# Kernel optimization log

Hardware: AMD Instinct MI355X
Metric: run time of the kernel (lower is better)

## Reference

```python
import jax, jax.numpy as jnp
import numpy as np
import math

EPS = 1e-5  # torch LayerNorm default


def entmax15(z):
    # Peters & Martins exact sort-based alpha=1.5 entmax along last axis.
    z = z / 2.0
    z = z - jnp.max(z, axis=-1, keepdims=True)
    zs = -jnp.sort(-z, axis=-1)                      # descending
    K = z.shape[-1]
    rho = jnp.arange(1, K + 1, dtype=z.dtype)
    mean = jnp.cumsum(zs, axis=-1) / rho
    mean_sq = jnp.cumsum(zs * zs, axis=-1) / rho
    ss = rho * (mean_sq - mean * mean)
    delta = jnp.clip((1.0 - ss) / rho, 0.0)
    tau = mean - jnp.sqrt(delta)
    k = jnp.sum(tau <= zs, axis=-1, keepdims=True)   # support size
    tau_star = jnp.take_along_axis(tau, k - 1, axis=-1)
    p = jnp.square(jnp.clip(z - tau_star, 0.0))
    return p


def mish(x):
    return x * jnp.tanh(jax.nn.softplus(x))


def layer_norm(x, g, b):
    mu = jnp.mean(x, axis=-1, keepdims=True)
    var = jnp.var(x, axis=-1, keepdims=True)
    return (x - mu) / jnp.sqrt(var + EPS) * g + b


def setup_inputs() -> dict:
    key = jax.random.key(0)
    D, H, F = 512, 8, 2048
    B, S = 8, 1024
    ks = jax.random.split(key, 16)
    s = 1.0 / math.sqrt(D)
    inp = {
        "x": jax.random.normal(ks[0], (B, S, D), jnp.float32),
        # weights stored [in, out]; y = x @ W + b
        "Wq": jax.random.normal(ks[1], (D, D), jnp.float32) * s,
        "bq": jnp.zeros((D,), jnp.float32),
        "Wk": jax.random.normal(ks[2], (D, D), jnp.float32) * s,
        "bk": jnp.zeros((D,), jnp.float32),
        "Wv": jax.random.normal(ks[3], (D, D), jnp.float32) * s,
        "bv": jnp.zeros((D,), jnp.float32),
        "Wo": jax.random.normal(ks[4], (D, D), jnp.float32) * s,
        "bo": jnp.zeros((D,), jnp.float32),
        "g1": jnp.ones((D,), jnp.float32),
        "be1": jnp.zeros((D,), jnp.float32),
        "W1": jax.random.normal(ks[5], (D, F), jnp.float32) * s,
        "b1": jnp.zeros((F,), jnp.float32),
        "W2": jax.random.normal(ks[6], (F, D), jnp.float32) * (1.0 / math.sqrt(F)),
        "b2": jnp.zeros((D,), jnp.float32),
        "g2": jnp.ones((D,), jnp.float32),
        "be2": jnp.zeros((D,), jnp.float32),
    }
    return inp


def reference(x, Wq, bq, Wk, bk, Wv, bv, Wo, bo, g1, be1, W1, b1, W2, b2, g2, be2):
    B, S, D = x.shape
    H = 8
    hd = D // H
    # multi-head self-attention (z = x)
    q = (x @ Wq + bq).reshape(B, S, H, hd).transpose(0, 2, 1, 3)
    k = (x @ Wk + bk).reshape(B, S, H, hd).transpose(0, 2, 1, 3)
    v = (x @ Wv + bv).reshape(B, S, H, hd).transpose(0, 2, 1, 3)
    scores = jnp.einsum("bhqd,bhkd->bhqk", q, k) / math.sqrt(hd)
    attn = entmax15(scores)
    out = jnp.einsum("bhqk,bhkd->bhqd", attn, v)
    out = out.transpose(0, 2, 1, 3).reshape(B, S, D)
    y = out @ Wo + bo
    x = x + layer_norm(y, g1, be1)
    # feed-forward with Mish
    y = mish(x @ W1 + b1) @ W2 + b2
    x = x + layer_norm(y, g2, be2)
    return x
```

## Files before the change

### kernel.cpp

```cpp
#include <hip/hip_runtime.h>


typedef float f32x4 __attribute__((ext_vector_type(4)));
typedef float f32x2 __attribute__((ext_vector_type(2)));
typedef __bf16 b8 __attribute__((ext_vector_type(8)));

#define DEV static __device__ __forceinline__

DEV unsigned short f2bf(float f) {
  unsigned u = __float_as_uint(f);
  u += 0x7fffu + ((u >> 16) & 1u);
  return (unsigned short)(u >> 16);
}
DEV float bf2f(unsigned short b) { return __uint_as_float(((unsigned)b) << 16); }

DEV float mishf(float x) {
  if (x > 20.f) return x;
  float e = __expf(x);
  float u = 1.f + e;
  u *= u;
  return x * ((u - 1.f) / (u + 1.f));
}

DEV void async16(const void* g, void* l) {
  __builtin_amdgcn_global_load_lds(
      (const __attribute__((address_space(1))) unsigned int*)g,
      (__attribute__((address_space(3))) unsigned int*)l, 16, 0, 0);
}

template <int WM, int WN, int EPI, bool OUTBF>
__global__ __launch_bounds__(256) void gemm_bt(
    const unsigned short* __restrict__ A, const unsigned short* __restrict__ Bt,
    const float* __restrict__ bias, void* __restrict__ Cp,
    int K, int lda, int ldb, int ldc,
    long sA1, long sA2, long sB1, long sB2, long sC1, long sC2,
    int hdiv, float alpha) {
  constexpr int BM = WM * 64, BN = WN * 64;
  constexpr int NA = WM * 2, NB = WN * 2;
  __shared__ unsigned short smA[BM * 64];
  __shared__ unsigned short smB[BN * 64];

  const int tid = threadIdx.x;
  const int lane = tid & 63;
  const int z = blockIdx.z;
  const long zi = z / hdiv, zr = z % hdiv;
  const unsigned short* Ab = A + zi * sA1 + zr * sA2 + (long)blockIdx.x * BM * lda;
  const unsigned short* Bb = Bt + zi * sB1 + zr * sB2 + (long)blockIdx.y * BN * ldb;

  int siA[NA];
  const unsigned short* gA[NA];
#pragma unroll
  for (int q = 0; q < NA; ++q) {
    int si = q * 256 + tid;
    int m = si >> 3, s = si & 7, g = s ^ (m & 7);
    siA[q] = si;
    gA[q] = Ab + (long)m * lda + g * 8;
  }
  int siB[NB];
  const unsigned short* gB[NB];
#pragma unroll
  for (int q = 0; q < NB; ++q) {
    int si = q * 256 + tid;
    int m = si >> 3, s = si & 7, g = s ^ (m & 7);
    siB[q] = si;
    gB[q] = Bb + (long)m * ldb + g * 8;
  }

  const int w = tid >> 6;
  const int wr = w / WN, wc = w % WN;
  const int fm = lane & 15, fg = lane >> 4;

  int aOff[4][2], bOff[4][2];
#pragma unroll
  for (int i = 0; i < 4; ++i)
#pragma unroll
    for (int ks = 0; ks < 2; ++ks) {
      int m = wr * 64 + i * 16 + fm;
      aOff[i][ks] = (m * 8 + ((ks * 4 + fg) ^ (fm & 7))) * 8;
      int n = wc * 64 + i * 16 + fm;
      bOff[i][ks] = (n * 8 + ((ks * 4 + fg) ^ (fm & 7))) * 8;
    }

  f32x4 acc[4][4];
#pragma unroll
  for (int i = 0; i < 4; ++i)
#pragma unroll
    for (int j = 0; j < 4; ++j) acc[i][j] = (f32x4){0.f, 0.f, 0.f, 0.f};

  for (int k0 = 0; k0 < K; k0 += 64) {
    __syncthreads();
#pragma unroll
    for (int q = 0; q < NA; ++q) async16(gA[q] + k0, (void*)&smA[siA[q] * 8]);
#pragma unroll
    for (int q = 0; q < NB; ++q) async16(gB[q] + k0, (void*)&smB[siB[q] * 8]);
    __syncthreads();

#pragma unroll
    for (int ks = 0; ks < 2; ++ks) {
      b8 aF[4], bF[4];
#pragma unroll
      for (int i = 0; i < 4; ++i) aF[i] = *(const b8*)&smA[aOff[i][ks]];
#pragma unroll
      for (int j = 0; j < 4; ++j) bF[j] = *(const b8*)&smB[bOff[j][ks]];
#pragma unroll
      for (int i = 0; i < 4; ++i)
#pragma unroll
        for (int j = 0; j < 4; ++j)
          acc[i][j] = __builtin_amdgcn_mfma_f32_16x16x32_bf16(aF[i], bF[j], acc[i][j], 0, 0, 0);
    }
  }

  const long cbase = zi * sC1 + zr * sC2;
  const int row0 = blockIdx.x * BM + wr * 64 + fg * 4;
  const int col0 = blockIdx.y * BN + wc * 64 + fm;
#pragma unroll
  for (int i = 0; i < 4; ++i) {
#pragma unroll
    for (int j = 0; j < 4; ++j) {
      const int col = col0 + j * 16;
      float bv = (EPI >= 1) ? bias[col] : 0.f;
#pragma unroll
      for (int r = 0; r < 4; ++r) {
        const int row = row0 + i * 16 + r;
        float v = acc[i][j][r] * alpha + bv;
        if (EPI == 2) v = mishf(v);
        const long idx = cbase + (long)row * ldc + col;
        if constexpr (OUTBF)
          ((unsigned short*)Cp)[idx] = f2bf(v);
        else
          ((float*)Cp)[idx] = v;
      }
    }
  }
}

__global__ __launch_bounds__(256) void entmax_rows(unsigned short* __restrict__ P) {
  const int tid = threadIdx.x, lane = tid & 63, wv = tid >> 6;
  const long row = (long)blockIdx.x * 4 + wv;
  unsigned short* p = P + row * 1024;

  union { uint4 v; unsigned short u[8]; } a, b;
  a.v = *(const uint4*)(p + lane * 16);
  b.v = *(const uint4*)(p + lane * 16 + 8);
  f32x2 zp[8];
#pragma unroll
  for (int i = 0; i < 4; ++i) {
    zp[i] = (f32x2){bf2f(a.u[2 * i]), bf2f(a.u[2 * i + 1])};
    zp[4 + i] = (f32x2){bf2f(b.u[2 * i]), bf2f(b.u[2 * i + 1])};
  }

  f32x2 mv = zp[0];
#pragma unroll
  for (int i = 1; i < 8; ++i) mv = __builtin_elementwise_max(mv, zp[i]);
  float m = fmaxf(mv.x, mv.y);
#pragma unroll
  for (int o = 32; o; o >>= 1) m = fmaxf(m, __shfl_xor(m, o));

  float tau = m - 1.f;
  int kprev = -1;
  const f32x2 zero2 = (f32x2){0.f, 0.f};
  for (int it = 0; it < 12; ++it) {
    const f32x2 t2 = (f32x2){tau, tau};
    f32x2 s1v = zero2, s2v = zero2;
    int k = 0;
#pragma unroll
    for (int i = 0; i < 8; ++i) {
      f32x2 h = zp[i] - t2;
      k += __popcll(__ballot(h.x > 0.f));
      k += __popcll(__ballot(h.y > 0.f));
      f32x2 hp = __builtin_elementwise_max(h, zero2);
      s1v += hp;
      s2v += hp * hp;
    }
    float s1 = s1v.x + s1v.y, s2 = s2v.x + s2v.y;
#pragma unroll
    for (int o = 32; o; o >>= 1) {
      s1 += __shfl_xor(s1, o);
      s2 += __shfl_xor(s2, o);
    }
    if (k == kprev) break;
    kprev = k;
    float kf = (float)k;
    float disc = fmaxf(fmaf(s1, s1, -kf * (s2 - 1.f)), 0.f);
    tau += (s1 - __builtin_sqrtf(disc)) / kf;
  }

  const f32x2 t2 = (f32x2){tau, tau};
#pragma unroll
  for (int i = 0; i < 4; ++i) {
    f32x2 h0 = __builtin_elementwise_max(zp[i] - t2, zero2);
    f32x2 h1 = __builtin_elementwise_max(zp[4 + i] - t2, zero2);
    f32x2 p0 = h0 * h0, p1 = h1 * h1;
    a.u[2 * i] = f2bf(p0.x);
    a.u[2 * i + 1] = f2bf(p0.y);
    b.u[2 * i] = f2bf(p1.x);
    b.u[2 * i + 1] = f2bf(p1.y);
  }
  *(uint4*)(p + lane * 16) = a.v;
  *(uint4*)(p + lane * 16 + 8) = b.v;
}

__global__ __launch_bounds__(256) void prep_all(
    const float* __restrict__ x, unsigned short* __restrict__ xb,
    const float* __restrict__ Wq, const float* __restrict__ Wk,
    const float* __restrict__ Wv, const float* __restrict__ Wo,
    const float* __restrict__ W1, const float* __restrict__ W2,
    unsigned short* __restrict__ Wqkvt, unsigned short* __restrict__ Wot,
    unsigned short* __restrict__ W1t, unsigned short* __restrict__ W2t,
    const float* __restrict__ bq, const float* __restrict__ bk,
    const float* __restrict__ bv, float* __restrict__ bqkv) {
  __shared__ float t[32][33];
  const int bid = blockIdx.x, tid = threadIdx.x;

  if (bid < 4096) {
    long i = ((long)bid * 256 + tid) * 4;
    float4 v = *(const float4*)&x[i];
    uint2 pk;
    pk.x = (unsigned)f2bf(v.x) | ((unsigned)f2bf(v.y) << 16);
    pk.y = (unsigned)f2bf(v.z) | ((unsigned)f2bf(v.w) << 16);
    *(uint2*)&xb[i] = pk;
    return;
  }

  const float* in;
  unsigned short* out;
  int ldi, ldo, bx, by;
  if (bid < 5120) {
    int t4 = (bid - 4096) >> 8, local = (bid - 4096) & 255;
    const float* ins[4] = {Wq, Wk, Wv, Wo};
    unsigned short* outs[4] = {Wqkvt, Wqkvt + 512 * 512, Wqkvt + 2 * 512 * 512, Wot};
    in = ins[t4];
    out = outs[t4];
    ldi = 512;
    ldo = 512;
    bx = local & 15;
    by = local >> 4;
  } else if (bid < 6144) {
    int local = bid - 5120;
    in = W1;
    out = W1t;
    ldi = 2048;
    ldo = 512;
    bx = local & 63;
    by = local >> 6;
  } else if (bid < 7168) {
    int local = bid - 6144;
    in = W2;
    out = W2t;
    ldi = 512;
    ldo = 2048;
    bx = local & 15;
    by = local >> 4;
  } else {
    int i = (bid - 7168) * 256 + tid;
    if (i < 512) bqkv[i] = bq[i];
    else if (i < 1024) bqkv[i] = bk[i - 512];
    else if (i < 1536) bqkv[i] = bv[i - 1024];
    return;
  }

  const int tx = tid & 31, ty = tid >> 5;
  const int r0 = by * 32, c0 = bx * 32;
#pragma unroll
  for (int q = 0; q < 4; ++q) {
    int r = ty + q * 8;
    t[r][tx] = in[(long)(r0 + r) * ldi + c0 + tx];
  }
  __syncthreads();
#pragma unroll
  for (int q = 0; q < 4; ++q) {
    int r = ty + q * 8;
    out[(long)(c0 + r) * ldo + r0 + tx] = f2bf(t[tx][r]);
  }
}

__global__ __launch_bounds__(256) void transpose_b2b(const unsigned short* __restrict__ in,
                                                     unsigned short* __restrict__ out,
                                                     int ldi, int ldo, long i1, long i2,
                                                     long o1, long o2, int hdiv) {
  __shared__ unsigned short t[32][33];
  const int z = blockIdx.z;
  in += (long)(z / hdiv) * i1 + (long)(z % hdiv) * i2;
  out += (long)(z / hdiv) * o1 + (long)(z % hdiv) * o2;
  const int tx = threadIdx.x & 31, ty = threadIdx.x >> 5;
  const int r0 = blockIdx.y * 32, c0 = blockIdx.x * 32;
#pragma unroll
  for (int q = 0; q < 4; ++q) {
    int r = ty + q * 8;
    t[r][tx] = in[(long)(r0 + r) * ldi + c0 + tx];
  }
  __syncthreads();
#pragma unroll
  for (int q = 0; q < 4; ++q) {
    int r = ty + q * 8;
    out[(long)(c0 + r) * ldo + r0 + tx] = t[tx][r];
  }
}

template <bool WB, int NS>
__global__ __launch_bounds__(256) void ln_res(const float* __restrict__ xin,
                                              const float* __restrict__ y, long ystr,
                                              const float* __restrict__ ybias,
                                              const float* __restrict__ g,
                                              const float* __restrict__ be,
                                              float* __restrict__ xo,
                                              unsigned short* __restrict__ xob) {
  const int row = blockIdx.x, tid = threadIdx.x, lane = tid & 63, wv = tid >> 6;
  const long base = (long)row * 512 + tid * 2;
  const int c = tid * 2;
  float2 v = *(const float2*)&y[base];
#pragma unroll
  for (int j = 1; j < NS; ++j) {
    float2 u = *(const float2*)&y[base + j * ystr];
    v.x += u.x;
    v.y += u.y;
  }
  v.x += ybias[c];
  v.y += ybias[c + 1];
  float s1 = v.x + v.y, s2 = v.x * v.x + v.y * v.y;
  for (int o = 32; o; o >>= 1) {
    s1 += __shfl_xor(s1, o);
    s2 += __shfl_xor(s2, o);
  }
  __shared__ float red[4][2];
  if (lane == 0) {
    red[wv][0] = s1;
    red[wv][1] = s2;
  }
  __syncthreads();
  s1 = red[0][0] + red[1][0] + red[2][0] + red[3][0];
  s2 = red[0][1] + red[1][1] + red[2][1] + red[3][1];
  const float mu = s1 * (1.f / 512.f);
  const float rstd = rsqrtf(s2 * (1.f / 512.f) - mu * mu + 1e-5f);
  float2 xv = *(const float2*)&xin[base];
  float o0 = xv.x + (v.x - mu) * rstd * g[c] + be[c];
  float o1 = xv.y + (v.y - mu) * rstd * g[c + 1] + be[c + 1];
  float2 ov;
  ov.x = o0;
  ov.y = o1;
  *(float2*)&xo[base] = ov;
  if constexpr (WB) {
    unsigned pk = (unsigned)f2bf(o0) | ((unsigned)f2bf(o1) << 16);
    *(unsigned*)&xob[base] = pk;
  }
}

extern "C" void kernel_launch(void* const* d_in, const int* in_sizes, int n_in,
                              void* d_out, int out_size, void* d_ws, size_t ws_size,
                              hipStream_t stream) {
  const int B = 8, S = 1024, D = 512, H = 8, F = 2048;
  const int BS = B * S;
  const int N3 = 3 * D;

  const float* x = (const float*)d_in[0];
  const float* Wq = (const float*)d_in[1];
  const float* bq = (const float*)d_in[2];
  const float* Wk = (const float*)d_in[3];
  const float* bk = (const float*)d_in[4];
  const float* Wv = (const float*)d_in[5];
  const float* bv = (const float*)d_in[6];
  const float* Wo = (const float*)d_in[7];
  const float* bo = (const float*)d_in[8];
  const float* g1 = (const float*)d_in[9];
  const float* be1 = (const float*)d_in[10];
  const float* W1 = (const float*)d_in[11];
  const float* b1 = (const float*)d_in[12];
  const float* W2 = (const float*)d_in[13];
  const float* b2 = (const float*)d_in[14];
  const float* g2 = (const float*)d_in[15];
  const float* be2 = (const float*)d_in[16];
  float* out = (float*)d_out;

  char* w = (char*)d_ws;
  size_t off = 0;
  auto alloc = [&](size_t bytes) -> void* {
    void* p = w + off;
    off += bytes;
    off = (off + 255) & ~(size_t)255;
    return p;
  };

  unsigned short* xb = (unsigned short*)alloc((size_t)BS * D * 2);
  unsigned short* Wqkvt = (unsigned short*)alloc((size_t)N3 * D * 2);
  unsigned short* Wot = (unsigned short*)alloc((size_t)D * D * 2);
  unsigned short* W1t = (unsigned short*)alloc((size_t)F * D * 2);
  unsigned short* W2t = (unsigned short*)alloc((size_t)D * F * 2);
  float* bqkv = (float*)alloc((size_t)N3 * 4);
  unsigned short* QKVb = (unsigned short*)alloc((size_t)BS * N3 * 2);
  unsigned short* Vt = (unsigned short*)alloc((size_t)BS * D * 2);
  unsigned short* attn = (unsigned short*)alloc((size_t)BS * D * 2);
  unsigned short* P = (unsigned short*)alloc((size_t)B * H * S * S * 2);
  float* x1 = (float*)alloc((size_t)BS * D * 4);
  unsigned short* hb = (unsigned short*)alloc((size_t)BS * F * 2);
  unsigned short* x1b = xb;
  float* yp = (float*)P;
  const long PSTR = (long)BS * D;

  const long SS = (long)S * S;
  const long HSS = (long)H * SS;

  prep_all<<<7174, 256, 0, stream>>>(x, xb, Wq, Wk, Wv, Wo, W1, W2,
                                     Wqkvt, Wot, W1t, W2t, bq, bk, bv, bqkv);

  gemm_bt<2, 2, 1, true><<<dim3(BS / 128, N3 / 128, 1), 256, 0, stream>>>(
      xb, Wqkvt, bqkv, QKVb, D, D, D, N3, 0, 0, 0, 0, 0, 0, 1, 1.f);

  transpose_b2b<<<dim3(2, 32, 64), 256, 0, stream>>>(
      QKVb + 1024, Vt, N3, S, (long)S * N3, 64, (long)8 * 64 * S, (long)64 * S, 8);

  gemm_bt<2, 2, 0, true><<<dim3(S / 128, S / 128, B * H), 256, 0, stream>>>(
      QKVb, QKVb + 512, nullptr, P, 64, N3, N3, S,
      (long)S * N3, 64, (long)S * N3, 64, HSS, SS, H, 1.f / 16.f);

  entmax_rows<<<(B * H * S) / 4, 256, 0, stream>>>(P);

  gemm_bt<4, 1, 0, true><<<dim3(S / 256, 1, B * H), 256, 0, stream>>>(
      P, Vt, nullptr, attn, S, S, S, D,
      HSS, SS, (long)8 * 64 * S, (long)64 * S, (long)S * D, 64, H, 1.f);

  gemm_bt<2, 2, 0, false><<<dim3(BS / 128, D / 128, 2), 256, 0, stream>>>(
      attn, Wot, nullptr, yp, D / 2, D, D, D, 0, D / 2, 0, D / 2, 0, PSTR, 2, 1.f);

  ln_res<true, 2><<<BS, 256, 0, stream>>>(x, yp, PSTR, bo, g1, be1, x1, x1b);

  gemm_bt<2, 2, 2, true><<<dim3(BS / 128, F / 128, 1), 256, 0, stream>>>(
      x1b, W1t, b1, hb, D, D, D, F, 0, 0, 0, 0, 0, 0, 1, 1.f);

  gemm_bt<2, 2, 0, false><<<dim3(BS / 128, D / 128, 2), 256, 0, stream>>>(
      hb, W2t, nullptr, yp, F / 2, F, F, D, 0, F / 2, 0, F / 2, 0, PSTR, 2, 1.f);

  ln_res<false, 2><<<BS, 256, 0, stream>>>(x1, yp, PSTR, b2, g2, be2, out, nullptr);
}
```

Before: 355.0 us.

## Swap GEMM operands to store 4-wide vectors; pack two entmax rows per wave

Every GEMM launch now computes the transposed product by swapping its A/B operands and grid axes. Each MFMA lane's four accumulator rows then map to contiguous output columns and can be written with one 8-byte or 16-byte store instead of four scalar stores. The bias is read as a float4 indexed by the new row dimension. The entmax kernel now handles two 1024-wide rows per wavefront, 32 lanes each, with per-half ballot counts and reductions, halving the block count and loading 32 elements per lane. Risks include the bias/layout remapping being correct only because of the swap, and the entmax loop running until both halves converge.

```diff
diff --git a/kernel.cpp b/kernel.cpp
--- a/kernel.cpp
+++ b/kernel.cpp
@@ -115,20 +115,33 @@
   const int col0 = blockIdx.y * BN + wc * 64 + fm;
 #pragma unroll
   for (int i = 0; i < 4; ++i) {
+    const int rowb = row0 + i * 16;
+    float4 bb = make_float4(0.f, 0.f, 0.f, 0.f);
+    if (EPI >= 1) bb = *(const float4*)&bias[rowb];
 #pragma unroll
     for (int j = 0; j < 4; ++j) {
       const int col = col0 + j * 16;
-      float bv = (EPI >= 1) ? bias[col] : 0.f;
-#pragma unroll
-      for (int r = 0; r < 4; ++r) {
-        const int row = row0 + i * 16 + r;
-        float v = acc[i][j][r] * alpha + bv;
-        if (EPI == 2) v = mishf(v);
-        const long idx = cbase + (long)row * ldc + col;
-        if constexpr (OUTBF)
-          ((unsigned short*)Cp)[idx] = f2bf(v);
-        else
-          ((float*)Cp)[idx] = v;
+      const long idx = cbase + (long)col * ldc + rowb;
+      float v0 = acc[i][j][0] * alpha + bb.x;
+      float v1 = acc[i][j][1] * alpha + bb.y;
+      float v2 = acc[i][j][2] * alpha + bb.z;
+      float v3 = acc[i][j][3] * alpha + bb.w;
+      if (EPI == 2) {
+        v0 = mishf(v0);
+        v1 = mishf(v1);
+        v2 = mishf(v2);
+        v3 = mishf(v3);
+      }
+      if constexpr (OUTBF) {
+        ushort4 pk;
+        pk.x = f2bf(v0);
+        pk.y = f2bf(v1);
+        pk.z = f2bf(v2);
+        pk.w = f2bf(v3);
+        *(ushort4*)&((unsigned short*)Cp)[idx] = pk;
+      } else {
+        float4 fv = make_float4(v0, v1, v2, v3);
+        *(float4*)&((float*)Cp)[idx] = fv;
       }
     }
   }
@@ -136,68 +149,71 @@
 
 __global__ __launch_bounds__(256) void entmax_rows(unsigned short* __restrict__ P) {
   const int tid = threadIdx.x, lane = tid & 63, wv = tid >> 6;
-  const long row = (long)blockIdx.x * 4 + wv;
-  unsigned short* p = P + row * 1024;
-
-  union { uint4 v; unsigned short u[8]; } a, b;
-  a.v = *(const uint4*)(p + lane * 16);
-  b.v = *(const uint4*)(p + lane * 16 + 8);
-  f32x2 zp[8];
-#pragma unroll
-  for (int i = 0; i < 4; ++i) {
-    zp[i] = (f32x2){bf2f(a.u[2 * i]), bf2f(a.u[2 * i + 1])};
-    zp[4 + i] = (f32x2){bf2f(b.u[2 * i]), bf2f(b.u[2 * i + 1])};
-  }
+  const int half = lane >> 5, l5 = lane & 31;
+  const long row = (long)blockIdx.x * 8 + wv * 2 + half;
+  unsigned short* p = P + row * 1024 + l5 * 32;
+
+  union { uint4 v; unsigned short u[8]; } t[4];
+#pragma unroll
+  for (int q = 0; q < 4; ++q) t[q].v = *(const uint4*)(p + q * 8);
+  f32x2 zp[16];
+#pragma unroll
+  for (int q = 0; q < 4; ++q)
+#pragma unroll
+    for (int i = 0; i < 4; ++i)
+      zp[q * 4 + i] = (f32x2){bf2f(t[q].u[2 * i]), bf2f(t[q].u[2 * i + 1])};
 
   f32x2 mv = zp[0];
 #pragma unroll
-  for (int i = 1; i < 8; ++i) mv = __builtin_elementwise_max(mv, zp[i]);
+  for (int i = 1; i < 16; ++i) mv = __builtin_elementwise_max(mv, zp[i]);
   float m = fmaxf(mv.x, mv.y);
 #pragma unroll
-  for (int o = 32; o; o >>= 1) m = fmaxf(m, __shfl_xor(m, o));
+  for (int o = 16; o; o >>= 1) m = fmaxf(m, __shfl_xor(m, o));
 
   float tau = m - 1.f;
-  int kprev = -1;
+  int kApr = -1, kBpr = -1;
   const f32x2 zero2 = (f32x2){0.f, 0.f};
   for (int it = 0; it < 12; ++it) {
     const f32x2 t2 = (f32x2){tau, tau};
     f32x2 s1v = zero2, s2v = zero2;
-    int k = 0;
-#pragma unroll
-    for (int i = 0; i < 8; ++i) {
+    int ka = 0, kb = 0;
+#pragma unroll
+    for (int i = 0; i < 16; ++i) {
       f32x2 h = zp[i] - t2;
-      k += __popcll(__ballot(h.x > 0.f));
-      k += __popcll(__ballot(h.y > 0.f));
+      unsigned long long b0 = __ballot(h.x > 0.f);
+      unsigned long long b1 = __ballot(h.y > 0.f);
+      ka += __popc((unsigned)b0) + __popc((unsigned)b1);
+      kb += __popc((unsigned)(b0 >> 32)) + __popc((unsigned)(b1 >> 32));
       f32x2 hp = __builtin_elementwise_max(h, zero2);
       s1v += hp;
       s2v += hp * hp;
     }
     float s1 = s1v.x + s1v.y, s2 = s2v.x + s2v.y;
 #pragma unroll
-    for (int o = 32; o; o >>= 1) {
+    for (int o = 16; o; o >>= 1) {
       s1 += __shfl_xor(s1, o);
       s2 += __shfl_xor(s2, o);
     }
-    if (k == kprev) break;
-    kprev = k;
-    float kf = (float)k;
+    if (ka == kApr && kb == kBpr) break;
+    kApr = ka;
+    kBpr = kb;
+    float kf = (float)(half ? kb : ka);
     float disc = fmaxf(fmaf(s1, s1, -kf * (s2 - 1.f)), 0.f);
     tau += (s1 - __builtin_sqrtf(disc)) / kf;
   }
 
   const f32x2 t2 = (f32x2){tau, tau};
 #pragma unroll
-  for (int i = 0; i < 4; ++i) {
-    f32x2 h0 = __builtin_elementwise_max(zp[i] - t2, zero2);
-    f32x2 h1 = __builtin_elementwise_max(zp[4 + i] - t2, zero2);
-    f32x2 p0 = h0 * h0, p1 = h1 * h1;
-    a.u[2 * i] = f2bf(p0.x);
-    a.u[2 * i + 1] = f2bf(p0.y);
-    b.u[2 * i] = f2bf(p1.x);
-    b.u[2 * i + 1] = f2bf(p1.y);
-  }
-  *(uint4*)(p + lane * 16) = a.v;
-  *(uint4*)(p + lane * 16 + 8) = b.v;
+  for (int q = 0; q < 4; ++q) {
+#pragma unroll
+    for (int i = 0; i < 4; ++i) {
+      f32x2 h = __builtin_elementwise_max(zp[q * 4 + i] - t2, zero2);
+      f32x2 pr = h * h;
+      t[q].u[2 * i] = f2bf(pr.x);
+      t[q].u[2 * i + 1] = f2bf(pr.y);
+    }
+    *(uint4*)(p + q * 8) = t[q].v;
+  }
 }
 
 __global__ __launch_bounds__(256) void prep_all(
@@ -398,36 +414,37 @@
 
   const long SS = (long)S * S;
   const long HSS = (long)H * SS;
+  const long SN3 = (long)S * N3;
 
   prep_all<<<7174, 256, 0, stream>>>(x, xb, Wq, Wk, Wv, Wo, W1, W2,
                                      Wqkvt, Wot, W1t, W2t, bq, bk, bv, bqkv);
 
-  gemm_bt<2, 2, 1, true><<<dim3(BS / 128, N3 / 128, 1), 256, 0, stream>>>(
-      xb, Wqkvt, bqkv, QKVb, D, D, D, N3, 0, 0, 0, 0, 0, 0, 1, 1.f);
+  gemm_bt<2, 2, 1, true><<<dim3(N3 / 128, BS / 128, 1), 256, 0, stream>>>(
+      Wqkvt, xb, bqkv, QKVb, D, D, D, N3, 0, 0, 0, 0, 0, 0, 1, 1.f);
 
   transpose_b2b<<<dim3(2, 32, 64), 256, 0, stream>>>(
-      QKVb + 1024, Vt, N3, S, (long)S * N3, 64, (long)8 * 64 * S, (long)64 * S, 8);
+      QKVb + 1024, Vt, N3, S, SN3, 64, (long)8 * 64 * S, (long)64 * S, 8);
 
   gemm_bt<2, 2, 0, true><<<dim3(S / 128, S / 128, B * H), 256, 0, stream>>>(
-      QKVb, QKVb + 512, nullptr, P, 64, N3, N3, S,
-      (long)S * N3, 64, (long)S * N3, 64, HSS, SS, H, 1.f / 16.f);
-
-  entmax_rows<<<(B * H * S) / 4, 256, 0, stream>>>(P);
-
-  gemm_bt<4, 1, 0, true><<<dim3(S / 256, 1, B * H), 256, 0, stream>>>(
-      P, Vt, nullptr, attn, S, S, S, D,
-      HSS, SS, (long)8 * 64 * S, (long)64 * S, (long)S * D, 64, H, 1.f);
-
-  gemm_bt<2, 2, 0, false><<<dim3(BS / 128, D / 128, 2), 256, 0, stream>>>(
-      attn, Wot, nullptr, yp, D / 2, D, D, D, 0, D / 2, 0, D / 2, 0, PSTR, 2, 1.f);
+      QKVb + 512, QKVb, nullptr, P, 64, N3, N3, S,
+      SN3, 64, SN3, 64, HSS, SS, H, 1.f / 16.f);
+
+  entmax_rows<<<(B * H * S) / 8, 256, 0, stream>>>(P);
+
+  gemm_bt<1, 4, 0, true><<<dim3(1, S / 256, B * H), 256, 0, stream>>>(
+      Vt, P, nullptr, attn, S, S, S, D,
+      (long)8 * 64 * S, (long)64 * S, HSS, SS, (long)S * D, 64, H, 1.f);
+
+  gemm_bt<2, 2, 0, false><<<dim3(D / 128, BS / 128, 2), 256, 0, stream>>>(
+      Wot, attn, nullptr, yp, D / 2, D, D, D, 0, D / 2, 0, D / 2, 0, PSTR, 2, 1.f);
 
   ln_res<true, 2><<<BS, 256, 0, stream>>>(x, yp, PSTR, bo, g1, be1, x1, x1b);
 
-  gemm_bt<2, 2, 2, true><<<dim3(BS / 128, F / 128, 1), 256, 0, stream>>>(
-      x1b, W1t, b1, hb, D, D, D, F, 0, 0, 0, 0, 0, 0, 1, 1.f);
-
-  gemm_bt<2, 2, 0, false><<<dim3(BS / 128, D / 128, 2), 256, 0, stream>>>(
-      hb, W2t, nullptr, yp, F / 2, F, F, D, 0, F / 2, 0, F / 2, 0, PSTR, 2, 1.f);
+  gemm_bt<2, 2, 2, true><<<dim3(F / 128, BS / 128, 1), 256, 0, stream>>>(
+      W1t, x1b, b1, hb, D, D, D, F, 0, 0, 0, 0, 0, 0, 1, 1.f);
+
+  gemm_bt<2, 2, 0, false><<<dim3(D / 128, BS / 128, 2), 256, 0, stream>>>(
+      W2t, hb, nullptr, yp, F / 2, F, F, D, 0, F / 2, 0, F / 2, 0, PSTR, 2, 1.f);
 
   ln_res<false, 2><<<BS, 256, 0, stream>>>(x1, yp, PSTR, b2, g2, be2, out, nullptr);
 }
```

Measured after the change: 388.0 us. 9.3% more time.
